# Kernel tuning notes

Measured on AMD Instinct MI355X. Metric: run time of the kernel, lower is better.

## Reference

```python
import jax, jax.numpy as jnp
import numpy as np

NUM_E = 100000
NUM_R = 500
HIDDEN = 64
BATCH = 32
GAMMA = 12.0
EPSILON = 2.0
EMB_RANGE = (GAMMA + EPSILON) / HIDDEN  # 0.21875
PI = 3.141592653589793


def setup_inputs() -> dict:
    key = jax.random.key(0)
    k1, k2, k3 = jax.random.split(key, 3)
    facts = jax.random.randint(k1, (BATCH, 3), 0, 1000, dtype=jnp.int64)  # col0<num_e, col1<2*num_r
    entity_embedding = jax.random.uniform(
        k2, (NUM_E, 2 * HIDDEN), dtype=jnp.float32, minval=-EMB_RANGE, maxval=EMB_RANGE)
    relation_embedding = jax.random.uniform(
        k3, (NUM_R * 2, HIDDEN), dtype=jnp.float32, minval=-EMB_RANGE, maxval=EMB_RANGE)
    return {"facts": facts, "entity_embedding": entity_embedding,
            "relation_embedding": relation_embedding}


def reference(facts, entity_embedding, relation_embedding):
    # Gather head/relation embeddings for the batch
    head = entity_embedding[facts[:, 0]]          # [B, 2D]
    relation = relation_embedding[facts[:, 1]]    # [B, D]

    re_head, im_head = jnp.split(head, 2, axis=1)           # [B, D] each
    re_tail, im_tail = jnp.split(entity_embedding, 2, axis=1)  # [E, D] each

    phase = relation / (EMB_RANGE / PI)
    re_rel = jnp.cos(phase)
    im_rel = jnp.sin(phase)

    # Complex rotation of head by relation: [B, D]
    re_rot = re_head * re_rel - im_head * im_rel
    im_rot = re_head * im_rel + im_head * re_rel

    # Broadcast difference against all entities: [B, E, D]
    re_diff = re_rot[:, None, :] - re_tail[None, :, :]
    im_diff = im_rot[:, None, :] - im_tail[None, :, :]

    # Per-component complex modulus, summed over dim -> [B, E]
    dist = jnp.sqrt(re_diff * re_diff + im_diff * im_diff).sum(axis=2)
    return GAMMA - dist
```

## Files before the change

### kernel.cpp

```cpp
#include <hip/hip_runtime.h>
#include <math.h>

#define NUM_E   100000
#define HIDDEN  64
#define BATCH   32
#define GAMMA_F 12.0f
#define EMB_RANGE_F 0.21875f
#define INV_TWO_EMB (1.0f / (2.0f * EMB_RANGE_F))

__global__ void rotate_phase_kernel(const int* __restrict__ facts,
                                    const float* __restrict__ ent,
                                    const float* __restrict__ rel,
                                    float* __restrict__ rot) {
    int p = blockIdx.x * blockDim.x + threadIdx.x;
    if (p >= BATCH * HIDDEN) return;
    int b = p >> 6;
    int d = p & 63;
    int f0 = facts[b * 3 + 0];
    int f1 = facts[b * 3 + 1];
    float hre = ent[(size_t)f0 * 128 + d];
    float him = ent[(size_t)f0 * 128 + 64 + d];
    float r   = rel[(size_t)f1 * 64 + d];
    float rev = r * INV_TWO_EMB;
    float s = __builtin_amdgcn_sinf(rev);
    float c = __builtin_amdgcn_cosf(rev);
    rot[p]                  = hre * c - him * s;
    rot[BATCH * HIDDEN + p] = hre * s + him * c;
}

__global__ __launch_bounds__(256) void rotate_dist_kernel(
        const float* __restrict__ ent,
        const float* __restrict__ rot,
        float* __restrict__ out) {
    __shared__ float s_rot[2 * BATCH * HIDDEN];
    {
        float4* s4 = (float4*)s_rot;
        const float4* r4 = (const float4*)rot;
        for (int i = threadIdx.x; i < (2 * BATCH * HIDDEN) / 4; i += 256)
            s4[i] = r4[i];
    }
    __syncthreads();

    const int g = threadIdx.x & 3;
    const int e = blockIdx.x * 64 + (threadIdx.x >> 2);
    const int e_c = (e < NUM_E) ? e : (NUM_E - 1);

    const float4* ent4 = (const float4*)(ent + (size_t)e_c * 128);

    float acc[BATCH];
#pragma unroll
    for (int b = 0; b < BATCH; ++b) acc[b] = 0.0f;

#pragma unroll 1
    for (int j = 0; j < 4; ++j) {
        const int dc = g + 4 * j;
        float4 tr = ent4[dc];
        float4 ti = ent4[16 + dc];
        const float4* rr4 = (const float4*)&s_rot[dc * 4];
        const float4* ri4 = (const float4*)&s_rot[BATCH * HIDDEN + dc * 4];
#pragma unroll
        for (int b = 0; b < BATCH; ++b) {
            float4 rr = rr4[b * (HIDDEN / 4)];
            float4 ri = ri4[b * (HIDDEN / 4)];
            float dx, dy;
            dx = rr.x - tr.x; dy = ri.x - ti.x;
            acc[b] += __builtin_amdgcn_sqrtf(dx * dx + dy * dy);
            dx = rr.y - tr.y; dy = ri.y - ti.y;
            acc[b] += __builtin_amdgcn_sqrtf(dx * dx + dy * dy);
            dx = rr.z - tr.z; dy = ri.z - ti.z;
            acc[b] += __builtin_amdgcn_sqrtf(dx * dx + dy * dy);
            dx = rr.w - tr.w; dy = ri.w - ti.w;
            acc[b] += __builtin_amdgcn_sqrtf(dx * dx + dy * dy);
        }
    }

#pragma unroll
    for (int b = 0; b < BATCH; ++b) {
        acc[b] += __shfl_xor(acc[b], 1, 64);
        acc[b] += __shfl_xor(acc[b], 2, 64);
    }

    if (e < NUM_E) {
#pragma unroll
        for (int b = 0; b < BATCH; ++b) {
            if ((b >> 3) == g)
                out[(size_t)b * NUM_E + e] = GAMMA_F - acc[b];
        }
    }
}

extern "C" void kernel_launch(void* const* d_in, const int* in_sizes, int n_in,
                              void* d_out, int out_size, void* d_ws, size_t ws_size,
                              hipStream_t stream) {
    const int*   facts = (const int*)d_in[0];
    const float* ent   = (const float*)d_in[1];
    const float* rel   = (const float*)d_in[2];
    float*       out   = (float*)d_out;
    float*       rot   = (float*)d_ws;

    rotate_phase_kernel<<<dim3((BATCH * HIDDEN + 255) / 256), dim3(256), 0, stream>>>(
        facts, ent, rel, rot);

    rotate_dist_kernel<<<dim3((NUM_E + 63) / 64), dim3(256), 0, stream>>>(
        ent, rot, out);
}
```

Baseline: 135.8 us.

## Keep rotated batch vectors in registers and map lanes to batch rows

The distance kernel no longer stages the rotated head vectors in shared memory. Each lane now holds half of one batch row's rotated real and imaginary parts in registers, and each wave loops over 8 entities. All lanes read the same entity row with broadcast loads, and the two halves are combined with a single cross-lane shuffle. This removes the LDS traffic, the block barrier and the 32-wide accumulator array, but each output store now writes 32 addresses spaced NUM_E apart, so writes are no longer coalesced.

```diff
diff --git a/kernel.cpp b/kernel.cpp
--- a/kernel.cpp
+++ b/kernel.cpp
@@ -7,6 +7,7 @@
 #define GAMMA_F 12.0f
 #define EMB_RANGE_F 0.21875f
 #define INV_TWO_EMB (1.0f / (2.0f * EMB_RANGE_F))
+#define NE 8
 
 __global__ void rotate_phase_kernel(const int* __restrict__ facts,
                                     const float* __restrict__ ent,
@@ -32,60 +33,51 @@
         const float* __restrict__ ent,
         const float* __restrict__ rot,
         float* __restrict__ out) {
-    __shared__ float s_rot[2 * BATCH * HIDDEN];
+    const int lane = threadIdx.x & 63;
+    const int wv   = threadIdx.x >> 6;
+    const int b    = lane & 31;
+    const int h    = lane >> 5;
+    const int gw   = blockIdx.x * 4 + wv;
+    const int e0   = gw * NE;
+
+    float4 RR[8], RI[8];
     {
-        float4* s4 = (float4*)s_rot;
-        const float4* r4 = (const float4*)rot;
-        for (int i = threadIdx.x; i < (2 * BATCH * HIDDEN) / 4; i += 256)
-            s4[i] = r4[i];
+        const float4* rr_p = (const float4*)(rot + b * 64 + h * 32);
+        const float4* ri_p = (const float4*)(rot + 2048 + b * 64 + h * 32);
+#pragma unroll
+        for (int c = 0; c < 8; ++c) { RR[c] = rr_p[c]; RI[c] = ri_p[c]; }
     }
-    __syncthreads();
-
-    const int g = threadIdx.x & 3;
-    const int e = blockIdx.x * 64 + (threadIdx.x >> 2);
-    const int e_c = (e < NUM_E) ? e : (NUM_E - 1);
-
-    const float4* ent4 = (const float4*)(ent + (size_t)e_c * 128);
-
-    float acc[BATCH];
-#pragma unroll
-    for (int b = 0; b < BATCH; ++b) acc[b] = 0.0f;
 
 #pragma unroll 1
-    for (int j = 0; j < 4; ++j) {
-        const int dc = g + 4 * j;
-        float4 tr = ent4[dc];
-        float4 ti = ent4[16 + dc];
-        const float4* rr4 = (const float4*)&s_rot[dc * 4];
-        const float4* ri4 = (const float4*)&s_rot[BATCH * HIDDEN + dc * 4];
+    for (int i = 0; i < NE; ++i) {
+        const int e = e0 + i;
+        const float4* tp = (const float4*)(ent + (size_t)e * 128 + h * 32);
+        const float4* ip = (const float4*)(ent + (size_t)e * 128 + 64 + h * 32);
+        float4 T[8], I[8];
 #pragma unroll
-        for (int b = 0; b < BATCH; ++b) {
-            float4 rr = rr4[b * (HIDDEN / 4)];
-            float4 ri = ri4[b * (HIDDEN / 4)];
-            float dx, dy;
-            dx = rr.x - tr.x; dy = ri.x - ti.x;
-            acc[b] += __builtin_amdgcn_sqrtf(dx * dx + dy * dy);
-            dx = rr.y - tr.y; dy = ri.y - ti.y;
-            acc[b] += __builtin_amdgcn_sqrtf(dx * dx + dy * dy);
-            dx = rr.z - tr.z; dy = ri.z - ti.z;
-            acc[b] += __builtin_amdgcn_sqrtf(dx * dx + dy * dy);
-            dx = rr.w - tr.w; dy = ri.w - ti.w;
-            acc[b] += __builtin_amdgcn_sqrtf(dx * dx + dy * dy);
+        for (int c = 0; c < 8; ++c) { T[c] = tp[c]; I[c] = ip[c]; }
+
+        float4 a4 = make_float4(0.f, 0.f, 0.f, 0.f);
+#pragma unroll
+        for (int c = 0; c < 8; ++c) {
+            float4 dx, dy, s;
+            dx.x = RR[c].x - T[c].x; dx.y = RR[c].y - T[c].y;
+            dx.z = RR[c].z - T[c].z; dx.w = RR[c].w - T[c].w;
+            dy.x = RI[c].x - I[c].x; dy.y = RI[c].y - I[c].y;
+            dy.z = RI[c].z - I[c].z; dy.w = RI[c].w - I[c].w;
+            s.x = dx.x * dx.x + dy.x * dy.x;
+            s.y = dx.y * dx.y + dy.y * dy.y;
+            s.z = dx.z * dx.z + dy.z * dy.z;
+            s.w = dx.w * dx.w + dy.w * dy.w;
+            a4.x += __builtin_amdgcn_sqrtf(s.x);
+            a4.y += __builtin_amdgcn_sqrtf(s.y);
+            a4.z += __builtin_amdgcn_sqrtf(s.z);
+            a4.w += __builtin_amdgcn_sqrtf(s.w);
         }
-    }
-
-#pragma unroll
-    for (int b = 0; b < BATCH; ++b) {
-        acc[b] += __shfl_xor(acc[b], 1, 64);
-        acc[b] += __shfl_xor(acc[b], 2, 64);
-    }
-
-    if (e < NUM_E) {
-#pragma unroll
-        for (int b = 0; b < BATCH; ++b) {
-            if ((b >> 3) == g)
-                out[(size_t)b * NUM_E + e] = GAMMA_F - acc[b];
-        }
+        float acc = (a4.x + a4.y) + (a4.z + a4.w);
+        acc += __shfl_xor(acc, 32, 64);
+        if (h == 0)
+            out[(size_t)b * NUM_E + e] = GAMMA_F - acc;
     }
 }
 
@@ -101,6 +93,6 @@
     rotate_phase_kernel<<<dim3((BATCH * HIDDEN + 255) / 256), dim3(256), 0, stream>>>(
         facts, ent, rel, rot);
 
-    rotate_dist_kernel<<<dim3((NUM_E + 63) / 64), dim3(256), 0, stream>>>(
+    rotate_dist_kernel<<<dim3(NUM_E / (NE * 4)), dim3(256), 0, stream>>>(
         ent, rot, out);
 }
```

After: 161.5 us. 19.0% more time.

## Keep rotated vectors in registers and stage entity tiles in LDS

Applied to the files above, without the earlier changes.

The distance kernel's data reuse is inverted. Each lane now holds its slice of the rotated head vectors (2 batches × 16 dims, real and imaginary) in registers. Each block stages 32 entity rows into shared memory, and every wave walks 8 entities, reducing partial sums across dimension groups with shuffles. This removes the repeated shared-memory reads of the full rotated batch for every entity. In exchange, output stores become scattered single-element writes across 32 batch rows, and register pressure rises (launch bounds now request 4 blocks).

```diff
diff --git a/kernel.cpp b/kernel.cpp
--- a/kernel.cpp
+++ b/kernel.cpp
@@ -7,6 +7,8 @@
 #define GAMMA_F 12.0f
 #define EMB_RANGE_F 0.21875f
 #define INV_TWO_EMB (1.0f / (2.0f * EMB_RANGE_F))
+
+typedef float v4f __attribute__((ext_vector_type(4)));
 
 __global__ void rotate_phase_kernel(const int* __restrict__ facts,
                                     const float* __restrict__ ent,
@@ -28,64 +30,69 @@
     rot[BATCH * HIDDEN + p] = hre * s + him * c;
 }
 
-__global__ __launch_bounds__(256) void rotate_dist_kernel(
+__global__ __launch_bounds__(256, 4) void rotate_dist_kernel(
         const float* __restrict__ ent,
         const float* __restrict__ rot,
         float* __restrict__ out) {
-    __shared__ float s_rot[2 * BATCH * HIDDEN];
+    __shared__ float s_ent[32 * 128];
+
+    const int t     = threadIdx.x;
+    const int tile0 = blockIdx.x * 32;
+
+    const int lane = t & 63;
+    const int wv   = t >> 6;
+    const int bg   = lane & 15;
+    const int dg   = lane >> 4;
+    v4f RR[2][4], RI[2][4];
+#pragma unroll
+    for (int kb = 0; kb < 2; ++kb) {
+        const int b = bg * 2 + kb;
+        const v4f* pr = (const v4f*)(rot + b * 64 + dg * 16);
+        const v4f* pi = (const v4f*)(rot + 2048 + b * 64 + dg * 16);
+#pragma unroll
+        for (int c = 0; c < 4; ++c) { RR[kb][c] = pr[c]; RI[kb][c] = pi[c]; }
+    }
+
     {
-        float4* s4 = (float4*)s_rot;
-        const float4* r4 = (const float4*)rot;
-        for (int i = threadIdx.x; i < (2 * BATCH * HIDDEN) / 4; i += 256)
-            s4[i] = r4[i];
+        const v4f* g4 = (const v4f*)(ent + (size_t)tile0 * 128);
+        v4f* s4 = (v4f*)s_ent;
+#pragma unroll
+        for (int j = 0; j < 4; ++j) s4[t + 256 * j] = g4[t + 256 * j];
     }
     __syncthreads();
 
-    const int g = threadIdx.x & 3;
-    const int e = blockIdx.x * 64 + (threadIdx.x >> 2);
-    const int e_c = (e < NUM_E) ? e : (NUM_E - 1);
+#pragma unroll 1
+    for (int i = 0; i < 8; ++i) {
+        const int e_local = wv * 8 + i;
+        const int e       = tile0 + e_local;
+        const v4f* pr = (const v4f*)(s_ent + e_local * 128 + dg * 16);
+        const v4f* pi = (const v4f*)(s_ent + e_local * 128 + 64 + dg * 16);
+        v4f er[4], ei[4];
+#pragma unroll
+        for (int c = 0; c < 4; ++c) { er[c] = pr[c]; ei[c] = pi[c]; }
 
-    const float4* ent4 = (const float4*)(ent + (size_t)e_c * 128);
-
-    float acc[BATCH];
+        float sum0, sum1;
 #pragma unroll
-    for (int b = 0; b < BATCH; ++b) acc[b] = 0.0f;
-
-#pragma unroll 1
-    for (int j = 0; j < 4; ++j) {
-        const int dc = g + 4 * j;
-        float4 tr = ent4[dc];
-        float4 ti = ent4[16 + dc];
-        const float4* rr4 = (const float4*)&s_rot[dc * 4];
-        const float4* ri4 = (const float4*)&s_rot[BATCH * HIDDEN + dc * 4];
+        for (int kb = 0; kb < 2; ++kb) {
+            v4f a = (v4f){0.f, 0.f, 0.f, 0.f};
 #pragma unroll
-        for (int b = 0; b < BATCH; ++b) {
-            float4 rr = rr4[b * (HIDDEN / 4)];
-            float4 ri = ri4[b * (HIDDEN / 4)];
-            float dx, dy;
-            dx = rr.x - tr.x; dy = ri.x - ti.x;
-            acc[b] += __builtin_amdgcn_sqrtf(dx * dx + dy * dy);
-            dx = rr.y - tr.y; dy = ri.y - ti.y;
-            acc[b] += __builtin_amdgcn_sqrtf(dx * dx + dy * dy);
-            dx = rr.z - tr.z; dy = ri.z - ti.z;
-            acc[b] += __builtin_amdgcn_sqrtf(dx * dx + dy * dy);
-            dx = rr.w - tr.w; dy = ri.w - ti.w;
-            acc[b] += __builtin_amdgcn_sqrtf(dx * dx + dy * dy);
+            for (int c = 0; c < 4; ++c) {
+                v4f dx = RR[kb][c] - er[c];
+                v4f dy = RI[kb][c] - ei[c];
+                v4f s  = dx * dx + dy * dy;
+                a.x += __builtin_amdgcn_sqrtf(s.x);
+                a.y += __builtin_amdgcn_sqrtf(s.y);
+                a.z += __builtin_amdgcn_sqrtf(s.z);
+                a.w += __builtin_amdgcn_sqrtf(s.w);
+            }
+            float sm = (a.x + a.y) + (a.z + a.w);
+            sm += __shfl_xor(sm, 16, 64);
+            sm += __shfl_xor(sm, 32, 64);
+            if (kb == 0) sum0 = sm; else sum1 = sm;
         }
-    }
-
-#pragma unroll
-    for (int b = 0; b < BATCH; ++b) {
-        acc[b] += __shfl_xor(acc[b], 1, 64);
-        acc[b] += __shfl_xor(acc[b], 2, 64);
-    }
-
-    if (e < NUM_E) {
-#pragma unroll
-        for (int b = 0; b < BATCH; ++b) {
-            if ((b >> 3) == g)
-                out[(size_t)b * NUM_E + e] = GAMMA_F - acc[b];
-        }
+        if (dg < 2)
+            out[(size_t)(bg * 2 + dg) * NUM_E + e] =
+                GAMMA_F - (dg == 0 ? sum0 : sum1);
     }
 }
 
@@ -101,6 +108,6 @@
     rotate_phase_kernel<<<dim3((BATCH * HIDDEN + 255) / 256), dim3(256), 0, stream>>>(
         facts, ent, rel, rot);
 
-    rotate_dist_kernel<<<dim3((NUM_E + 63) / 64), dim3(256), 0, stream>>>(
+    rotate_dist_kernel<<<dim3(NUM_E / 32), dim3(256), 0, stream>>>(
         ent, rot, out);
 }
```

After: 124.9 us. 1.09x faster.
